# Optimization experiments

Hardware: AMD Instinct MI355X
Metric: run time of the kernel (lower is better)

## Reference

```python
import jax, jax.numpy as jnp
import numpy as np

NUM_HEADS = 16
MASKED_BIAS = -10000.0


def setup_inputs() -> dict:
    key = jax.random.key(0)
    k1, k2, k3 = jax.random.split(key, 3)
    B, S, D = 4, 2048, 1024
    return {
        "hidden_states": jax.random.normal(k1, (B, S, D), dtype=jnp.float32),
        "attention_mask": jnp.ones((B, S), dtype=jnp.float32),
        "w_attn": jax.random.normal(k2, (D, 3 * D), dtype=jnp.float32) * 0.02,
        "b_attn": jax.random.normal(k3, (3 * D,), dtype=jnp.float32) * 0.1,
    }


def reference(hidden_states, attention_mask, w_attn, b_attn):
    B, S, D = hidden_states.shape
    H = NUM_HEADS
    Dh = D // H
    # Conv1D: x @ W + b  -> [B, S, 3D]
    qkv = hidden_states @ w_attn + b_attn
    q, k, v = jnp.split(qkv, 3, axis=-1)

    def split_heads(t):  # [B,S,D] -> [B,H,S,Dh]
        return t.reshape(B, S, H, Dh).transpose(0, 2, 1, 3)

    q, k, v = split_heads(q), split_heads(k), split_heads(v)
    present = jnp.stack([k, v], axis=0)  # concat_key_value

    # process_mask: (1 - mask) * -10000, broadcast [B,1,1,S]
    add_mask = (1.0 - attention_mask)[:, None, None, :] * MASKED_BIAS

    qk = jnp.einsum("bhqd,bhkd->bhqk", q, k)
    norm_qk = qk * (1.0 / float(Dh) ** 0.5)
    causal = jnp.tril(jnp.ones((S, S), dtype=bool))[None, None]
    attn_weights = jnp.where(causal, norm_qk, jnp.asarray(MASKED_BIAS, norm_qk.dtype))
    attn_weights = attn_weights + add_mask
    probs = jax.nn.softmax(attn_weights, axis=-1)
    attn_output = jnp.einsum("bhqk,bhkd->bhqd", probs, v)
    # merge heads -> [B,S,D]
    attn_output = attn_output.transpose(0, 2, 1, 3).reshape(B, S, D)
    return attn_output, present
```

## Files before the change

### kernel.cpp

```cpp
#include <hip/hip_runtime.h>
#include <stdint.h>


#define B_SZ    4
#define S_LEN   2048
#define D_MODEL 1024
#define N3      3072
#define H_NUM   16
#define DH      64
#define M_TOT   8192

typedef __attribute__((ext_vector_type(8))) short short8;
typedef __attribute__((ext_vector_type(4))) short bf16x4;
typedef __attribute__((ext_vector_type(4))) float f32x4;

#define LOG2E      1.4426950408889634f
#define SCL2E      0.18033688011112042f
#define MASKB2     (-14426.9504f)

__device__ __forceinline__ unsigned short f2b(float f) {
  union { float f; unsigned int u; } x;
  x.f = f;
  unsigned int u = x.u;
  u += 0x7fffu + ((u >> 16) & 1u);
  return (unsigned short)(u >> 16);
}

__device__ __forceinline__ unsigned int cvt_pk_bf16(float lo, float hi) {
  unsigned int r;
  asm("v_cvt_pk_bf16_f32 %0, %1, %2" : "=v"(r) : "v"(lo), "v"(hi));
  return r;
}

__device__ __forceinline__ float exp2_fast(float x) {
#if __has_builtin(__builtin_amdgcn_exp2f)
  return __builtin_amdgcn_exp2f(x);
#else
  return __expf(x * 0.6931471805599453f);
#endif
}

__device__ __forceinline__ f32x4 mfma16(bf16x4 a, bf16x4 b, f32x4 c) {
#if __has_builtin(__builtin_amdgcn_mfma_f32_16x16x16bf16_1k)
  return __builtin_amdgcn_mfma_f32_16x16x16bf16_1k(a, b, c, 0, 0, 0);
#else
  asm("v_mfma_f32_16x16x16_bf16 %0, %1, %2, %0" : "+v"(c) : "v"(a), "v"(b));
  return c;
#endif
}

__device__ __forceinline__ void async16(const void* g, void* l) {
  __builtin_amdgcn_global_load_lds((const __attribute__((address_space(1))) void*)g,
                                   (__attribute__((address_space(3))) void*)l,
                                   16, 0, 0);
}

__global__ void k_convert_x(const float* __restrict__ X, unsigned short* __restrict__ Xb) {
  const int i = (blockIdx.x * 256 + threadIdx.x) * 4;
  const float4 v = *(const float4*)(X + i);
  ushort4 o;
  o.x = f2b(v.x); o.y = f2b(v.y); o.z = f2b(v.z); o.w = f2b(v.w);
  *(ushort4*)(Xb + i) = o;
}

__global__ void k_wt(const float* __restrict__ W, unsigned short* __restrict__ Wt) {
  __shared__ float tile[32][33];
  const int n0 = blockIdx.x * 32, k0 = blockIdx.y * 32;
  const int tx = threadIdx.x, ty = threadIdx.y;
  for (int i = 0; i < 32; i += 8)
    tile[ty + i][tx] = W[(size_t)(k0 + ty + i) * N3 + n0 + tx];
  __syncthreads();
  for (int i = 0; i < 32; i += 8)
    Wt[(size_t)(n0 + ty + i) * D_MODEL + k0 + tx] = f2b(tile[tx][ty + i]);
}

__global__ __launch_bounds__(256) void k_gemm_qkv(
    const unsigned short* __restrict__ Xb, const unsigned short* __restrict__ Wt,
    const float* __restrict__ bias,
    unsigned short* __restrict__ Qb, unsigned short* __restrict__ Kb,
    float* __restrict__ presK, float* __restrict__ presV) {
  __shared__ __align__(16) unsigned short SMEM[8192];
  unsigned short* As = SMEM;
  unsigned short* Bs = SMEM + 4096;
  const int t = threadIdx.x;
  const int lane = t & 63, wave = t >> 6;
  const int g = lane >> 4, c = lane & 15;
  const int m0 = blockIdx.y * 128, n0 = blockIdx.x * 128;
  const int wm = (wave >> 1) * 64, wn = (wave & 1) * 64;

  const f32x4 zero = {0.f, 0.f, 0.f, 0.f};
  f32x4 acc[4][4];
  for (int i = 0; i < 4; ++i)
    for (int j = 0; j < 4; ++j) acc[i][j] = zero;

  const int row_a = t >> 2;
  const int col_a = (t & 3) * 8;
  const unsigned short* gA = Xb + (size_t)(m0 + row_a) * D_MODEL + col_a;
  const unsigned short* gB = Wt + (size_t)(n0 + row_a) * D_MODEL + col_a;
  const int wbase = wave * 1024;

  for (int k0 = 0; k0 < D_MODEL; k0 += 32) {
    __syncthreads();
    async16(gA + k0,                (char*)As + wbase);
    async16(gA + k0 + 64 * D_MODEL, (char*)As + 4096 + wbase);
    async16(gB + k0,                (char*)Bs + wbase);
    async16(gB + k0 + 64 * D_MODEL, (char*)Bs + 4096 + wbase);
    __syncthreads();

    short8 af[4], bf[4];
    for (int mi = 0; mi < 4; ++mi)
      af[mi] = *(const short8*)(As + (wm + mi * 16 + c) * 32 + g * 8);
    for (int ni = 0; ni < 4; ++ni)
      bf[ni] = *(const short8*)(Bs + (wn + ni * 16 + c) * 32 + g * 8);
    for (int mi = 0; mi < 4; ++mi)
      for (int ni = 0; ni < 4; ++ni)
        acc[mi][ni] = __builtin_amdgcn_mfma_f32_16x16x32_bf16(af[mi], bf[ni], acc[mi][ni], 0, 0, 0);
  }

  __syncthreads();

  const int sec = (n0 + wn) >> 10;
  const int h = ((n0 + wn) & 1023) >> 6;
  unsigned short* slab = SMEM + wave * 1152;
  float bv[4];
  for (int ni = 0; ni < 4; ++ni) bv[ni] = bias[n0 + wn + ni * 16 + c];

  for (int mi = 0; mi < 4; ++mi) {
    const int mrow = m0 + wm + mi * 16;

    if (sec != 2) {
      for (int ni = 0; ni < 4; ++ni)
        for (int r = 0; r < 4; ++r)
          slab[(g * 4 + r) * 72 + ni * 16 + c] = f2b(acc[mi][ni][r] + bv[ni]);
      const short8 w0 = *(const short8*)(slab + c * 72 + g * 16);
      const short8 w1 = *(const short8*)(slab + c * 72 + g * 16 + 8);
      const int srow = mrow + c;
      const int b = srow >> 11, s = srow & 2047;
      unsigned short* dst = (sec == 0 ? Qb : Kb) +
          ((size_t)((b * H_NUM + h) * S_LEN + s)) * DH + g * 16;
      *(short8*)(dst) = w0;
      *(short8*)(dst + 8) = w1;
    }
    if (sec >= 1) {
      float* dstf = (sec == 1) ? presK : presV;
      for (int ni = 0; ni < 4; ++ni) {
        const int dh = ni * 16 + c;
        for (int r = 0; r < 4; ++r) {
          const int m = mrow + g * 4 + r;
          const int b = m >> 11, s = m & 2047;
          dstf[((size_t)((b * H_NUM + h) * S_LEN + s)) * DH + dh] =
              acc[mi][ni][r] + bv[ni];
        }
      }
    }
  }
}

__global__ __launch_bounds__(256) void k_vt(const float* __restrict__ presV,
                                            unsigned short* __restrict__ Vt) {
  __shared__ unsigned short tile[64 * 72];
  const int t = threadIdx.x;
  const int bh = blockIdx.y;
  const int s0 = blockIdx.x * 64;
  const int row = t >> 2;
  const int dh0 = (t & 3) * 16;
  const float* src = presV + ((size_t)bh * S_LEN + s0 + row) * DH + dh0;
  for (int i = 0; i < 4; ++i) {
    const float4 v = *(const float4*)(src + i * 4);
    const int dh = dh0 + i * 4;
    tile[(dh + 0) * 72 + row] = f2b(v.x);
    tile[(dh + 1) * 72 + row] = f2b(v.y);
    tile[(dh + 2) * 72 + row] = f2b(v.z);
    tile[(dh + 3) * 72 + row] = f2b(v.w);
  }
  __syncthreads();
  const int dh = t >> 2, p0 = (t & 3) * 16;
  unsigned short* dst = Vt + ((size_t)bh * DH + dh) * S_LEN + s0 + p0;
  short8 o0, o1;
  for (int i = 0; i < 8; ++i) {
    const int pa = p0 + i, pb = p0 + 8 + i;
    const int ka = (((pa >> 2) & 3) << 4) | (((pa >> 4) & 3) << 2) | (pa & 3);
    const int kb = (((pb >> 2) & 3) << 4) | (((pb >> 4) & 3) << 2) | (pb & 3);
    o0[i] = (short)tile[dh * 72 + ka];
    o1[i] = (short)tile[dh * 72 + kb];
  }
  *(short8*)(dst) = o0;
  *(short8*)(dst + 8) = o1;
}

#define PROC_SET(BQ, QR, NC, MI, LI, OA, PK)                                \
  {                                                                         \
    f32x4 sc[4];                                                            \
    _Pragma("unroll")                                                       \
    for (int ks = 0; ks < 4; ++ks) {                                        \
      f32x4 a = zero;                                                       \
      const int krow = ks * 16 + c;                                         \
      _Pragma("unroll")                                                     \
      for (int kc = 0; kc < 2; ++kc) {                                      \
        const short8 ak = *(const short8*)(ks_base + krow * 64 +            \
                                           (((kc * 4 + g) ^ kslot) * 8));   \
        a = __builtin_amdgcn_mfma_f32_16x16x32_bf16(ak, BQ[kc], a, 0, 0, 0);\
      }                                                                     \
      sc[ks] = a;                                                           \
    }                                                                       \
    float mx = -3.0e38f;                                                    \
    _Pragma("unroll")                                                       \
    for (int ks = 0; ks < 4; ++ks) {                                        \
      _Pragma("unroll")                                                     \
      for (int r = 0; r < 4; ++r) {                                         \
        float v = sc[ks][r] * SCL2E + amf[ks][r];                           \
        if (NC && (kb + ks * 16 + g * 4 + r > (QR))) v = MASKB2 + amf[ks][r];\
        sc[ks][r] = v;                                                      \
      }                                                                     \
      mx = fmaxf(mx, fmaxf(fmaxf(sc[ks][0], sc[ks][1]),                     \
                           fmaxf(sc[ks][2], sc[ks][3])));                   \
    }                                                                       \
    mx = fmaxf(mx, __shfl_xor(mx, 16));                                     \
    mx = fmaxf(mx, __shfl_xor(mx, 32));                                     \
    if (!__all(mx <= MI + 8.0f)) {                                          \
      const float mnew = fmaxf(MI, mx);                                     \
      const float alpha = exp2_fast(MI - mnew);                             \
      MI = mnew;                                                            \
      LI *= alpha;                                                          \
      _Pragma("unroll")                                                     \
      for (int dt = 0; dt < 4; ++dt) OA[dt] *= alpha;                       \
    }                                                                       \
    float rs = 0.f;                                                         \
    _Pragma("unroll")                                                       \
    for (int ks = 0; ks < 4; ++ks) {                                        \
      const float p0 = exp2_fast(sc[ks][0] - MI);                           \
      const float p1 = exp2_fast(sc[ks][1] - MI);                           \
      const float p2 = exp2_fast(sc[ks][2] - MI);                           \
      const float p3 = exp2_fast(sc[ks][3] - MI);                           \
      rs += (p0 + p1) + (p2 + p3);                                          \
      union { unsigned int u[2]; bf16x4 v4; } pu;                           \
      pu.u[0] = cvt_pk_bf16(p0, p1);                                        \
      pu.u[1] = cvt_pk_bf16(p2, p3);                                        \
      PK[ks] = pu.v4;                                                       \
    }                                                                       \
    rs += __shfl_xor(rs, 16);                                               \
    rs += __shfl_xor(rs, 32);                                               \
    LI += rs;                                                               \
  }

__global__ __launch_bounds__(512) void k_flash(
    const unsigned short* __restrict__ Qb, const unsigned short* __restrict__ Kb,
    const unsigned short* __restrict__ Vt, const float* __restrict__ mask,
    float* __restrict__ out) {
  __shared__ __align__(16) unsigned short Ks[2][64 * 64];
  __shared__ __align__(16) unsigned short Vs[2][64 * 64];
  __shared__ __align__(16) float Ams[S_LEN];
  const int t = threadIdx.x;
  const int lane = t & 63, wave = t >> 6;
  const int g = lane >> 4, c = lane & 15;
  const int bh = blockIdx.x;
  const int b = bh >> 4, h = bh & 15;
  const int srow = t >> 3;
  const int schunk = (t & 7) ^ (srow & 7);
  const unsigned short* gK0 = Kb + ((size_t)bh * S_LEN + srow) * DH + schunk * 8;
  const unsigned short* gV0 = Vt + ((size_t)bh * DH + srow) * S_LEN + schunk * 8;
  const int kslot = c & 7;

  {
    const float4 mv = *(const float4*)(mask + (size_t)b * S_LEN + t * 4);
    float4 o;
    o.x = (1.0f - mv.x) * MASKB2;
    o.y = (1.0f - mv.y) * MASKB2;
    o.z = (1.0f - mv.z) * MASKB2;
    o.w = (1.0f - mv.w) * MASKB2;
    *(float4*)(Ams + t * 4) = o;
  }

  const f32x4 zero = {0.f, 0.f, 0.f, 0.f};

  const int qb = (7 - (int)blockIdx.y) * 256;
  const int qw = qb + wave * 32;
  const int qrA = qw + c;
  const int qrB = qw + 16 + c;

  short8 bqA[2], bqB[2];
  {
    const size_t qoff = ((size_t)bh * S_LEN + qw) * DH;
#pragma unroll
    for (int kc = 0; kc < 2; ++kc) {
      bqA[kc] = *(const short8*)(Qb + qoff + (size_t)c * DH + kc * 32 + g * 8);
      bqB[kc] = *(const short8*)(Qb + qoff + (size_t)(c + 16) * DH + kc * 32 + g * 8);
    }
  }

  float m_iA = -1e30f, l_iA = 0.f, m_iB = -1e30f, l_iB = 0.f;
  f32x4 o_A[4], o_B[4];
#pragma unroll
  for (int dt = 0; dt < 4; ++dt) { o_A[dt] = zero; o_B[dt] = zero; }

  const int nt = (qb + 256) >> 6;
  async16(gK0, (char*)(&Ks[0][0]) + wave * 1024);
  async16(gV0, (char*)(&Vs[0][0]) + wave * 1024);

  for (int tt = 0; tt < nt; ++tt) {
    const int kb = tt << 6;
    const int cur = tt & 1;
    if (tt + 1 < nt) {
      async16(gK0 + (size_t)(kb + 64) * DH, (char*)(&Ks[cur ^ 1][0]) + wave * 1024);
      async16(gV0 + (kb + 64),              (char*)(&Vs[cur ^ 1][0]) + wave * 1024);
      asm volatile("s_waitcnt vmcnt(2) lgkmcnt(0)" ::: "memory");
    } else {
      asm volatile("s_waitcnt vmcnt(0) lgkmcnt(0)" ::: "memory");
    }
    __builtin_amdgcn_s_barrier();
    __builtin_amdgcn_sched_barrier(0);

    if (qw + 32 > kb) {
      const unsigned short* ks_base = &Ks[cur][0];
      const unsigned short* vs_base = &Vs[cur][0];

      float amf[4][4];
#pragma unroll
      for (int ks = 0; ks < 4; ++ks) {
        const float4 amv = *(const float4*)(Ams + kb + ks * 16 + g * 4);
        amf[ks][0] = amv.x; amf[ks][1] = amv.y;
        amf[ks][2] = amv.z; amf[ks][3] = amv.w;
      }
      const bool ncA = (kb + 63 > qw);
      const bool ncB = (kb + 63 > qw + 16);

      bf16x4 pkA[4], pkB[4];
      PROC_SET(bqA, qrA, ncA, m_iA, l_iA, o_A, pkA)
      PROC_SET(bqB, qrB, ncB, m_iB, l_iB, o_B, pkB)

#pragma unroll
      for (int dt = 0; dt < 4; ++dt) {
        const int vrow = dt * 16 + c;
#pragma unroll
        for (int jp = 0; jp < 2; ++jp) {
          union { short8 s8; bf16x4 h[2]; } vv;
          vv.s8 = *(const short8*)(vs_base + vrow * 64 + (((2 * g + jp) ^ kslot) * 8));
          o_A[dt] = mfma16(vv.h[0], pkA[2 * jp], o_A[dt]);
          o_A[dt] = mfma16(vv.h[1], pkA[2 * jp + 1], o_A[dt]);
          o_B[dt] = mfma16(vv.h[0], pkB[2 * jp], o_B[dt]);
          o_B[dt] = mfma16(vv.h[1], pkB[2 * jp + 1], o_B[dt]);
        }
      }
    }
    __builtin_amdgcn_sched_barrier(0);
    __builtin_amdgcn_s_barrier();
  }

  {
    const float inv = 1.0f / l_iA;
    float* orow = out + ((size_t)(b * S_LEN + qrA)) * D_MODEL + h * DH;
#pragma unroll
    for (int dt = 0; dt < 4; ++dt) {
      float4 o;
      o.x = o_A[dt][0] * inv;
      o.y = o_A[dt][1] * inv;
      o.z = o_A[dt][2] * inv;
      o.w = o_A[dt][3] * inv;
      *(float4*)(orow + dt * 16 + g * 4) = o;
    }
  }
  {
    const float inv = 1.0f / l_iB;
    float* orow = out + ((size_t)(b * S_LEN + qrB)) * D_MODEL + h * DH;
#pragma unroll
    for (int dt = 0; dt < 4; ++dt) {
      float4 o;
      o.x = o_B[dt][0] * inv;
      o.y = o_B[dt][1] * inv;
      o.z = o_B[dt][2] * inv;
      o.w = o_B[dt][3] * inv;
      *(float4*)(orow + dt * 16 + g * 4) = o;
    }
  }
}

extern "C" void kernel_launch(void* const* d_in, const int* in_sizes, int n_in,
                              void* d_out, int out_size, void* d_ws, size_t ws_size,
                              hipStream_t stream) {
  const float* X    = (const float*)d_in[0];
  const float* mask = (const float*)d_in[1];
  const float* W    = (const float*)d_in[2];
  const float* bias = (const float*)d_in[3];

  float* out   = (float*)d_out;
  float* presK = out + (size_t)M_TOT * D_MODEL;
  float* presV = presK + (size_t)M_TOT * D_MODEL;

  char* ws = (char*)d_ws;
  unsigned short* Xb = (unsigned short*)(ws);
  unsigned short* Wt = (unsigned short*)(ws + 16777216);
  unsigned short* Qb = (unsigned short*)(ws + 23068672);
  unsigned short* Kb = (unsigned short*)(ws + 39845888);
  unsigned short* Vt = (unsigned short*)(ws + 56623104);

  k_convert_x<<<dim3(8192), dim3(256), 0, stream>>>(X, Xb);
  k_wt<<<dim3(96, 32), dim3(32, 8), 0, stream>>>(W, Wt);
  k_gemm_qkv<<<dim3(24, 64), dim3(256), 0, stream>>>(Xb, Wt, bias, Qb, Kb, presK, presV);
  k_vt<<<dim3(32, 64), dim3(256), 0, stream>>>(presV, Vt);
  k_flash<<<dim3(64, 8), dim3(512), 0, stream>>>(Qb, Kb, Vt, mask, out);
}
```

Before: 296.1 us.

## Pair causal query tiles per block for balanced work with 256-thread blocks

```diff
diff --git a/kernel.cpp b/kernel.cpp
--- a/kernel.cpp
+++ b/kernel.cpp
@@ -243,7 +243,7 @@
     LI += rs;                                                               \
   }
 
-__global__ __launch_bounds__(512) void k_flash(
+__global__ __launch_bounds__(256) void k_flash(
     const unsigned short* __restrict__ Qb, const unsigned short* __restrict__ Kb,
     const unsigned short* __restrict__ Vt, const float* __restrict__ mask,
     float* __restrict__ out) {
@@ -253,7 +253,7 @@
   const int t = threadIdx.x;
   const int lane = t & 63, wave = t >> 6;
   const int g = lane >> 4, c = lane & 15;
-  const int bh = blockIdx.x;
+  const int bh = blockIdx.y;
   const int b = bh >> 4, h = bh & 15;
   const int srow = t >> 3;
   const int schunk = (t & 7) ^ (srow & 7);
@@ -262,114 +262,124 @@
   const int kslot = c & 7;
 
   {
-    const float4 mv = *(const float4*)(mask + (size_t)b * S_LEN + t * 4);
-    float4 o;
-    o.x = (1.0f - mv.x) * MASKB2;
-    o.y = (1.0f - mv.y) * MASKB2;
-    o.z = (1.0f - mv.z) * MASKB2;
-    o.w = (1.0f - mv.w) * MASKB2;
-    *(float4*)(Ams + t * 4) = o;
+    const float4 mv0 = *(const float4*)(mask + (size_t)b * S_LEN + t * 8);
+    const float4 mv1 = *(const float4*)(mask + (size_t)b * S_LEN + t * 8 + 4);
+    float4 o0, o1;
+    o0.x = (1.0f - mv0.x) * MASKB2; o0.y = (1.0f - mv0.y) * MASKB2;
+    o0.z = (1.0f - mv0.z) * MASKB2; o0.w = (1.0f - mv0.w) * MASKB2;
+    o1.x = (1.0f - mv1.x) * MASKB2; o1.y = (1.0f - mv1.y) * MASKB2;
+    o1.z = (1.0f - mv1.z) * MASKB2; o1.w = (1.0f - mv1.w) * MASKB2;
+    *(float4*)(Ams + t * 8) = o0;
+    *(float4*)(Ams + t * 8 + 4) = o1;
   }
 
   const f32x4 zero = {0.f, 0.f, 0.f, 0.f};
 
-  const int qb = (7 - (int)blockIdx.y) * 256;
-  const int qw = qb + wave * 32;
-  const int qrA = qw + c;
-  const int qrB = qw + 16 + c;
-
-  short8 bqA[2], bqB[2];
-  {
-    const size_t qoff = ((size_t)bh * S_LEN + qw) * DH;
-#pragma unroll
-    for (int kc = 0; kc < 2; ++kc) {
-      bqA[kc] = *(const short8*)(Qb + qoff + (size_t)c * DH + kc * 32 + g * 8);
-      bqB[kc] = *(const short8*)(Qb + qoff + (size_t)(c + 16) * DH + kc * 32 + g * 8);
-    }
-  }
-
-  float m_iA = -1e30f, l_iA = 0.f, m_iB = -1e30f, l_iB = 0.f;
-  f32x4 o_A[4], o_B[4];
-#pragma unroll
-  for (int dt = 0; dt < 4; ++dt) { o_A[dt] = zero; o_B[dt] = zero; }
-
-  const int nt = (qb + 256) >> 6;
-  async16(gK0, (char*)(&Ks[0][0]) + wave * 1024);
-  async16(gV0, (char*)(&Vs[0][0]) + wave * 1024);
-
-  for (int tt = 0; tt < nt; ++tt) {
-    const int kb = tt << 6;
-    const int cur = tt & 1;
-    if (tt + 1 < nt) {
-      async16(gK0 + (size_t)(kb + 64) * DH, (char*)(&Ks[cur ^ 1][0]) + wave * 1024);
-      async16(gV0 + (kb + 64),              (char*)(&Vs[cur ^ 1][0]) + wave * 1024);
-      asm volatile("s_waitcnt vmcnt(2) lgkmcnt(0)" ::: "memory");
-    } else {
-      asm volatile("s_waitcnt vmcnt(0) lgkmcnt(0)" ::: "memory");
-    }
-    __builtin_amdgcn_s_barrier();
-    __builtin_amdgcn_sched_barrier(0);
-
-    if (qw + 32 > kb) {
-      const unsigned short* ks_base = &Ks[cur][0];
-      const unsigned short* vs_base = &Vs[cur][0];
-
-      float amf[4][4];
-#pragma unroll
-      for (int ks = 0; ks < 4; ++ks) {
-        const float4 amv = *(const float4*)(Ams + kb + ks * 16 + g * 4);
-        amf[ks][0] = amv.x; amf[ks][1] = amv.y;
-        amf[ks][2] = amv.z; amf[ks][3] = amv.w;
-      }
-      const bool ncA = (kb + 63 > qw);
-      const bool ncB = (kb + 63 > qw + 16);
-
-      bf16x4 pkA[4], pkB[4];
-      PROC_SET(bqA, qrA, ncA, m_iA, l_iA, o_A, pkA)
-      PROC_SET(bqB, qrB, ncB, m_iB, l_iB, o_B, pkB)
-
+  for (int phase = 0; phase < 2; ++phase) {
+    const int x = phase ? 15 - (int)blockIdx.x : (int)blockIdx.x;
+    const int qb = x * 128;
+    const int qw = qb + wave * 32;
+    const int qrA = qw + c;
+    const int qrB = qw + 16 + c;
+
+    short8 bqA[2], bqB[2];
+    {
+      const size_t qoff = ((size_t)bh * S_LEN + qw) * DH;
+#pragma unroll
+      for (int kc = 0; kc < 2; ++kc) {
+        bqA[kc] = *(const short8*)(Qb + qoff + (size_t)c * DH + kc * 32 + g * 8);
+        bqB[kc] = *(const short8*)(Qb + qoff + (size_t)(c + 16) * DH + kc * 32 + g * 8);
+      }
+    }
+
+    float m_iA = -1e30f, l_iA = 0.f, m_iB = -1e30f, l_iB = 0.f;
+    f32x4 o_A[4], o_B[4];
+#pragma unroll
+    for (int dt = 0; dt < 4; ++dt) { o_A[dt] = zero; o_B[dt] = zero; }
+
+    const int nt = (qb + 128) >> 6;
+    async16(gK0,               (char*)(&Ks[0][0]) + wave * 1024);
+    async16(gK0 + 32 * DH,     (char*)(&Ks[0][0]) + 4096 + wave * 1024);
+    async16(gV0,               (char*)(&Vs[0][0]) + wave * 1024);
+    async16(gV0 + 32 * S_LEN,  (char*)(&Vs[0][0]) + 4096 + wave * 1024);
+
+    for (int tt = 0; tt < nt; ++tt) {
+      const int kb = tt << 6;
+      const int cur = tt & 1;
+      if (tt + 1 < nt) {
+        const size_t ko = (size_t)(kb + 64) * DH;
+        async16(gK0 + ko,                   (char*)(&Ks[cur ^ 1][0]) + wave * 1024);
+        async16(gK0 + ko + 32 * DH,         (char*)(&Ks[cur ^ 1][0]) + 4096 + wave * 1024);
+        async16(gV0 + kb + 64,              (char*)(&Vs[cur ^ 1][0]) + wave * 1024);
+        async16(gV0 + kb + 64 + 32 * S_LEN, (char*)(&Vs[cur ^ 1][0]) + 4096 + wave * 1024);
+        asm volatile("s_waitcnt vmcnt(4) lgkmcnt(0)" ::: "memory");
+      } else {
+        asm volatile("s_waitcnt vmcnt(0) lgkmcnt(0)" ::: "memory");
+      }
+      __builtin_amdgcn_s_barrier();
+      __builtin_amdgcn_sched_barrier(0);
+
+      if (qw + 32 > kb) {
+        const unsigned short* ks_base = &Ks[cur][0];
+        const unsigned short* vs_base = &Vs[cur][0];
+
+        float amf[4][4];
+#pragma unroll
+        for (int ks = 0; ks < 4; ++ks) {
+          const float4 amv = *(const float4*)(Ams + kb + ks * 16 + g * 4);
+          amf[ks][0] = amv.x; amf[ks][1] = amv.y;
+          amf[ks][2] = amv.z; amf[ks][3] = amv.w;
+        }
+        const bool ncA = (kb + 63 > qw);
+        const bool ncB = (kb + 63 > qw + 16);
+
+        bf16x4 pkA[4], pkB[4];
+        PROC_SET(bqA, qrA, ncA, m_iA, l_iA, o_A, pkA)
+        PROC_SET(bqB, qrB, ncB, m_iB, l_iB, o_B, pkB)
+
+#pragma unroll
+        for (int dt = 0; dt < 4; ++dt) {
+          const int vrow = dt * 16 + c;
+#pragma unroll
+          for (int jp = 0; jp < 2; ++jp) {
+            union { short8 s8; bf16x4 hh[2]; } vv;
+            vv.s8 = *(const short8*)(vs_base + vrow * 64 + (((2 * g + jp) ^ kslot) * 8));
+            o_A[dt] = mfma16(vv.hh[0], pkA[2 * jp], o_A[dt]);
+            o_A[dt] = mfma16(vv.hh[1], pkA[2 * jp + 1], o_A[dt]);
+            o_B[dt] = mfma16(vv.hh[0], pkB[2 * jp], o_B[dt]);
+            o_B[dt] = mfma16(vv.hh[1], pkB[2 * jp + 1], o_B[dt]);
+          }
+        }
+      }
+      __builtin_amdgcn_sched_barrier(0);
+      __builtin_amdgcn_s_barrier();
+    }
+
+    {
+      const float inv = 1.0f / l_iA;
+      float* orow = out + ((size_t)(b * S_LEN + qrA)) * D_MODEL + h * DH;
 #pragma unroll
       for (int dt = 0; dt < 4; ++dt) {
-        const int vrow = dt * 16 + c;
-#pragma unroll
-        for (int jp = 0; jp < 2; ++jp) {
-          union { short8 s8; bf16x4 h[2]; } vv;
-          vv.s8 = *(const short8*)(vs_base + vrow * 64 + (((2 * g + jp) ^ kslot) * 8));
-          o_A[dt] = mfma16(vv.h[0], pkA[2 * jp], o_A[dt]);
-          o_A[dt] = mfma16(vv.h[1], pkA[2 * jp + 1], o_A[dt]);
-          o_B[dt] = mfma16(vv.h[0], pkB[2 * jp], o_B[dt]);
-          o_B[dt] = mfma16(vv.h[1], pkB[2 * jp + 1], o_B[dt]);
-        }
-      }
-    }
-    __builtin_amdgcn_sched_barrier(0);
-    __builtin_amdgcn_s_barrier();
-  }
-
-  {
-    const float inv = 1.0f / l_iA;
-    float* orow = out + ((size_t)(b * S_LEN + qrA)) * D_MODEL + h * DH;
-#pragma unroll
-    for (int dt = 0; dt < 4; ++dt) {
-      float4 o;
-      o.x = o_A[dt][0] * inv;
-      o.y = o_A[dt][1] * inv;
-      o.z = o_A[dt][2] * inv;
-      o.w = o_A[dt][3] * inv;
-      *(float4*)(orow + dt * 16 + g * 4) = o;
-    }
-  }
-  {
-    const float inv = 1.0f / l_iB;
-    float* orow = out + ((size_t)(b * S_LEN + qrB)) * D_MODEL + h * DH;
-#pragma unroll
-    for (int dt = 0; dt < 4; ++dt) {
-      float4 o;
-      o.x = o_B[dt][0] * inv;
-      o.y = o_B[dt][1] * inv;
-      o.z = o_B[dt][2] * inv;
-      o.w = o_B[dt][3] * inv;
-      *(float4*)(orow + dt * 16 + g * 4) = o;
+        float4 o;
+        o.x = o_A[dt][0] * inv;
+        o.y = o_A[dt][1] * inv;
+        o.z = o_A[dt][2] * inv;
+        o.w = o_A[dt][3] * inv;
+        *(float4*)(orow + dt * 16 + g * 4) = o;
+      }
+    }
+    {
+      const float inv = 1.0f / l_iB;
+      float* orow = out + ((size_t)(b * S_LEN + qrB)) * D_MODEL + h * DH;
+#pragma unroll
+      for (int dt = 0; dt < 4; ++dt) {
+        float4 o;
+        o.x = o_B[dt][0] * inv;
+        o.y = o_B[dt][1] * inv;
+        o.z = o_B[dt][2] * inv;
+        o.w = o_B[dt][3] * inv;
+        *(float4*)(orow + dt * 16 + g * 4) = o;
+      }
     }
   }
 }
@@ -397,5 +407,5 @@
   k_wt<<<dim3(96, 32), dim3(32, 8), 0, stream>>>(W, Wt);
   k_gemm_qkv<<<dim3(24, 64), dim3(256), 0, stream>>>(Xb, Wt, bias, Qb, Kb, presK, presV);
   k_vt<<<dim3(32, 64), dim3(256), 0, stream>>>(presV, Vt);
-  k_flash<<<dim3(64, 8), dim3(512), 0, stream>>>(Qb, Kb, Vt, mask, out);
-}
+  k_flash<<<dim3(8, 64), dim3(256), 0, stream>>>(Qb, Kb, Vt, mask, out);
+}
```

Result: no change. 298.2 us (+0.7%).
